# Optimization experiments

Measured on AMD Instinct MI355X. Metric: run time of the kernel, lower is better.

## Reference

```python
import jax, jax.numpy as jnp
import numpy as np

D = 128          # node_embedding_dim
R = 1024         # num_root_nodes
T = 4            # num trunk node types; encoder index T is the output autoencoder
OUT_SLOTS = 256  # num_output_nodes
START = T        # output_node_types_start
L = 64           # topological levels after the roots
M = 2048         # nodes per level
N = R + L * M    # total nodes = 132096


def setup_inputs() -> dict:
    key = jax.random.key(0)
    ks = jax.random.split(key, 4)
    rng = np.random.default_rng(0)
    # DAG by topological level: node in level l (1-based) reads parents with index < R + (l-1)*M
    hi = np.repeat(R + np.arange(L) * M, M)  # (N-R,) exclusive upper bound per node
    par = (rng.random((N - R, 2)) * hi[:, None]).astype(np.int64)
    is_out = rng.random(N - R) < 0.05
    types = rng.integers(0, T, N - R)
    types = np.where(is_out, START + rng.integers(0, OUT_SLOTS, N - R), types).astype(np.int64)
    s = 1.0 / np.sqrt(2 * D)
    return {
        "root_node_embeddings": jax.random.normal(ks[0], (R, D), jnp.float32),
        "W1": jax.random.normal(ks[1], (T + 1, 2 * D, 2 * D), jnp.float32) * s,  # encoder layer 1 (in, out)
        "b1": jnp.zeros((T + 1, 2 * D), jnp.float32),
        "W2": jax.random.normal(ks[2], (T + 1, 2 * D, D), jnp.float32) * s,      # encoder layer 2
        "b2": jnp.zeros((T + 1, D), jnp.float32),
        "out_slot_emb": jax.random.normal(ks[3], (OUT_SLOTS, D), jnp.float32),   # output_node_embeddings.weight
        "node_inputs_indices": jnp.asarray(par),  # (N-R, 2)
        "node_types": jnp.asarray(types),         # (N-R,)
    }


def _evaluate_graph(root, W1, b1, W2, b2, slots, par_idx, types):
    buf0 = jnp.zeros((N, D), root.dtype).at[:R].set(root)
    par_l = par_idx.reshape(L, M, 2)
    typ_l = types.reshape(L, M)
    m_ar = jnp.arange(M)

    def level_step(buf, inp):
        l, par, t = inp                        # par: (M,2) parent indices, t: (M,) node types
        is_out = t >= START
        e_idx = jnp.where(is_out, T, t)        # which autoencoder per node
        slot = jnp.clip(t - START, 0, OUT_SLOTS - 1)
        p = buf[par]                           # (M, 2, D) gather parent embeddings
        # output nodes use [parent0, slot_embedding] as encode input
        p1 = jnp.where(is_out[:, None], slots[slot], p[:, 1])
        x = jnp.concatenate([p[:, 0], p1], axis=-1)  # (M, 2D) flattened encoder input
        # run all T+1 tiny encoders, pick each node's type (cheap: weights are tiny)
        h_all = jnp.einsum('mi,tio->tmo', x, W1) + b1[:, None, :]  # (T+1, M, 2D)
        h = jax.nn.gelu(h_all[e_idx, m_ar], approximate=False)     # (M, 2D) exact GELU (torch default)
        e_all = jnp.einsum('mi,tio->tmo', h, W2) + b2[:, None, :]  # (T+1, M, D)
        e = e_all[e_idx, m_ar]                                     # (M, D)
        buf = jax.lax.dynamic_update_slice(buf, e, (R + l * M, 0))  # scatter level results
        return buf, None

    buf, _ = jax.lax.scan(level_step, buf0, (jnp.arange(L), par_l, typ_l))
    return buf


_evaluate_graph_jit = jax.jit(_evaluate_graph)


def reference(root_node_embeddings, W1, b1, W2, b2, out_slot_emb, node_inputs_indices, node_types):
    return _evaluate_graph_jit(root_node_embeddings, W1, b1, W2, b2, out_slot_emb,
                               node_inputs_indices, node_types)
```

## Files before the change

### kernel.cpp

```cpp
#include <hip/hip_runtime.h>
#include <math.h>

#define DD 128
#define RR 1024
#define TT 4
#define LL 64
#define MM 2048
#define NBK 16
#define GT 37
#define GO 10
#define CCAP (4*GT + GO)
#define PAD16 (CCAP*NBK)
#define CH CCAP
#define SENTU 0xFFFFFFFFu

typedef __attribute__((ext_vector_type(8))) short short8v;
typedef __attribute__((ext_vector_type(4))) float f32x4;

static __device__ __forceinline__ unsigned short f2bf(float f) {
    unsigned u = __float_as_uint(f);
    unsigned r = (u + 0x7fffu + ((u >> 16) & 1u)) >> 16;
    return (unsigned short)r;
}

static __device__ __forceinline__ float gelu_f(float h) {
    float x  = h * 0.70710678118654752f;
    float ax = fabsf(x);
    float t  = __builtin_amdgcn_rcpf(fmaf(0.3275911f, ax, 1.0f));
    float p  = fmaf(t, 1.061405429f, -1.453152027f);
    p = fmaf(p, t, 1.421413741f);
    p = fmaf(p, t, -0.284496736f);
    p = fmaf(p, t, 0.254829592f);
    p = p * t;
    float er = 1.0f - p * __expf(-ax * ax);
    er = copysignf(er, x);
    return 0.5f * h * (1.0f + er);
}

__global__ __launch_bounds__(256) void prep_all(
    const float* __restrict__ root, const float* __restrict__ W1,
    const float* __restrict__ W2, const int* __restrict__ types,
    const int* __restrict__ par,
    float* __restrict__ buf,
    unsigned short* __restrict__ W1F, unsigned short* __restrict__ W2F,
    unsigned short* __restrict__ order)
{
    int bid = blockIdx.x, tid = threadIdx.x;
    if (bid < LL) {
        int l = bid;
        __shared__ int cnt[10], cur[10];
        if (tid < 10) cnt[tid] = 0;
        __syncthreads();
        for (int s = tid; s < PAD16; s += 256) order[l*PAD16 + s] = 0xFFFFu;
        int thr = RR + (l-1)*MM;
        for (int m = tid; m < MM; m += 256) {
            int gi = l*MM + m;
            int t = types[gi];
            int e = (t >= TT) ? TT : t;
            int p0 = par[2*gi];
            bool rec = (p0 >= RR) && (p0 >= thr);
            if (t < TT) {
                int p1 = par[2*gi + 1];
                rec = rec || ((p1 >= RR) && (p1 >= thr));
            }
            atomicAdd(&cnt[e*2 + (rec ? 1 : 0)], 1);
        }
        __syncthreads();
        if (tid == 0) {
            for (int e = 0; e < 5; e++) {
                int base = ((e < 4) ? e*GT : 4*GT) * NBK;
                int s = cnt[e*2];
                cur[e*2]     = base;
                cur[e*2 + 1] = base + ((s + NBK - 1)/NBK)*NBK;
            }
        }
        __syncthreads();
        for (int m = tid; m < MM; m += 256) {
            int gi = l*MM + m;
            int t = types[gi];
            int e = (t >= TT) ? TT : t;
            int p0 = par[2*gi];
            bool rec = (p0 >= RR) && (p0 >= thr);
            if (t < TT) {
                int p1 = par[2*gi + 1];
                rec = rec || ((p1 >= RR) && (p1 >= thr));
            }
            int pos = atomicAdd(&cur[e*2 + (rec ? 1 : 0)], 1);
            order[l*PAD16 + pos] = (unsigned short)m;
        }
    } else if (bid < LL + 240) {
        int t0 = (bid - LL)*256 + tid;
        if (t0 < 5*16*8*64) {
            int lane = t0 & 63;
            int kk = (t0 >> 6) & 7;
            int nt = (t0 >> 9) & 15;
            int e  = t0 >> 13;
            int n  = nt*16 + (lane & 15);
            int k0 = kk*32 + (lane >> 4)*8;
            unsigned short v[8];
            #pragma unroll
            for (int j = 0; j < 8; j++) v[j] = f2bf(W1[(e*256 + k0 + j)*256 + n]);
            *(short8v*)&W1F[t0*8] = *(short8v*)v;
        } else {
            int t = t0 - 5*16*8*64;
            int lane = t & 63;
            int kk = (t >> 6) & 7;
            int nt = (t >> 9) & 7;
            int e  = t >> 12;
            int n  = nt*16 + (lane & 15);
            int k0 = kk*32 + (lane >> 4)*8;
            unsigned short v[8];
            #pragma unroll
            for (int j = 0; j < 8; j++) v[j] = f2bf(W2[(e*256 + k0 + j)*128 + n]);
            *(short8v*)&W2F[t*8] = *(short8v*)v;
        }
    } else if (bid < LL + 240 + 32) {
        int idx = (bid - (LL + 240))*256 + tid;
        const f32x4* r4 = (const f32x4*)root;
        f32x4* o4 = (f32x4*)buf;
        #pragma unroll
        for (int q = 0; q < 4; q++) o4[idx*4 + q] = r4[idx*4 + q];
    } else {
        int idx = (bid - (LL + 240 + 32))*256 + tid;
        float s = __uint_as_float(SENTU);
        f32x4 sv = (f32x4){s, s, s, s};
        f32x4* p = (f32x4*)(buf + (size_t)RR*DD) + (size_t)idx*4;
        p[0] = sv; p[1] = sv; p[2] = sv; p[3] = sv;
    }
}

__global__ __launch_bounds__(512, 2) void persist_mfma(
    const unsigned short* __restrict__ W1F, const unsigned short* __restrict__ W2F,
    const float* __restrict__ b1, const float* __restrict__ b2,
    const float* __restrict__ slots, const int* __restrict__ par,
    const int* __restrict__ types, const unsigned short* __restrict__ order,
    float* __restrict__ buf)
{
    __shared__ int4 descs[LL][NBK];
    __shared__ int ech[LL];
    __shared__ unsigned short axFA[8*64*8];
    __shared__ unsigned short axFB[8*64*8];
    __shared__ unsigned short hxF[8*64*8];

    int tid = threadIdx.x;
    int wg  = blockIdx.x;
    int e_wg = (wg < 4*GT) ? (wg / GT) : TT;

    int w  = tid >> 6;
    int lq = tid & 63;
    int m_own   = tid >> 4;
    int seg_own = tid & 15;

    short8v w1r0[8], w1r1[8], w2r[8];
    #pragma unroll
    for (int kk = 0; kk < 8; kk++) {
        w1r0[kk] = *(const short8v*)&W1F[(((e_wg*16 + 2*w + 0)*8 + kk)*64 + lq)*8];
        w1r1[kk] = *(const short8v*)&W1F[(((e_wg*16 + 2*w + 1)*8 + kk)*64 + lq)*8];
        w2r[kk]  = *(const short8v*)&W2F[(((e_wg*8  + w)*8 + kk)*64 + lq)*8];
    }
    float b1v0 = b1[e_wg*256 + (2*w + 0)*16 + (lq & 15)];
    float b1v1 = b1[e_wg*256 + (2*w + 1)*16 + (lq & 15)];
    float b2v  = b2[e_wg*128 + w*16 + (lq & 15)];

    for (int i = tid; i < LL*NBK; i += 512) {
        int l = i >> 4, s = i & 15;
        unsigned short o = order[l*PAD16 + wg*NBK + s];
        int4 d;
        if (o == 0xFFFFu) {
            d = make_int4(-1, 0, 0, -1);
        } else {
            int gi = l*MM + (int)o;
            int t = types[gi];
            int e = (t >= TT) ? TT : t;
            int p0 = par[2*gi];
            int p1 = (t >= TT) ? ~(t - TT) : par[2*gi + 1];
            d = make_int4((int)o, p0, p1, e);
        }
        descs[l][s] = d;
    }
    __syncthreads();
    for (int i = tid; i < LL; i += 512) ech[i] = descs[i][0].w;
    __syncthreads();

    #define RESOLVE_SRC(l1, S, P) {                                            \
        int4 d_ = descs[l1][m_own];                                            \
        if (d_.x < 0) { P = true; S = nullptr; }                               \
        else {                                                                 \
            P = false;                                                         \
            if (seg_own < 8)   S = buf + (size_t)d_.y*DD + seg_own*16;         \
            else if (d_.z < 0) S = slots + (size_t)(~d_.z)*DD + (seg_own-8)*16;\
            else               S = buf + (size_t)d_.z*DD + (seg_own-8)*16;     \
        } }

    #define LOAD8(S, U) {                                                      \
        const unsigned long long* s8_ = (const unsigned long long*)(S);        \
        _Pragma("unroll")                                                      \
        for (int q_ = 0; q_ < 8; q_++)                                         \
            U[q_] = __hip_atomic_load(&s8_[q_], __ATOMIC_RELAXED,              \
                                      __HIP_MEMORY_SCOPE_AGENT);               \
    }

    #define VERIFY(U, OK) { OK = true;                                         \
        _Pragma("unroll")                                                      \
        for (int q_ = 0; q_ < 8; q_++) {                                       \
            unsigned lo_ = (unsigned)U[q_], hi_ = (unsigned)(U[q_] >> 32);     \
            OK = OK && (lo_ != SENTU) && (hi_ != SENTU);                       \
        } }

    #define WRITE_FRAGS_U(AXT, U) {                                            \
        unsigned short tA_[8], tB_[8];                                         \
        _Pragma("unroll")                                                      \
        for (int q_ = 0; q_ < 4; q_++) {                                       \
            tA_[2*q_]   = f2bf(__uint_as_float((unsigned)U[q_]));              \
            tA_[2*q_+1] = f2bf(__uint_as_float((unsigned)(U[q_] >> 32)));      \
            tB_[2*q_]   = f2bf(__uint_as_float((unsigned)U[4+q_]));            \
            tB_[2*q_+1] = f2bf(__uint_as_float((unsigned)(U[4+q_] >> 32)));    \
        }                                                                      \
        int k_ = seg_own*16;                                                   \
        int kk_ = k_ >> 5, ln_ = m_own + 16*((k_ >> 3) & 3);                   \
        *(short8v*)&AXT[(kk_*64 + ln_)*8] = *(short8v*)tA_;                    \
        k_ += 8; kk_ = k_ >> 5; ln_ = m_own + 16*((k_ >> 3) & 3);              \
        *(short8v*)&AXT[(kk_*64 + ln_)*8] = *(short8v*)tB_;                    \
    }

    if (tid < 256) {
        const float* src; bool pad;
        RESOLVE_SRC(0, src, pad);
        unsigned long long u0[8];
        if (!pad) {
            LOAD8(src, u0);
            bool ok; VERIFY(u0, ok);
            while (!ok) { __builtin_amdgcn_s_sleep(1); LOAD8(src, u0); VERIFY(u0, ok); }
        } else {
            #pragma unroll
            for (int q = 0; q < 8; q++) u0[q] = 0ull;
        }
        WRITE_FRAGS_U(axFA, u0);
    }
    __syncthreads();

    unsigned short* axc = axFA;
    unsigned short* axn = axFB;

    for (int l = 0; l < LL; l++) {
        bool havN = (l + 1 < LL);

        const float* srcN = nullptr; bool padN = true; bool ok = true;
        unsigned long long u[8];
        #pragma unroll
        for (int q = 0; q < 8; q++) u[q] = 0ull;
        if (havN && tid < 256) {
            RESOLVE_SRC(l+1, srcN, padN);
            if (!padN) { LOAD8(srcN, u); ok = false; }
        }
        __builtin_amdgcn_sched_barrier(0);

        int e = ech[l];
        if (e >= 0) {
            f32x4 acc0 = (f32x4){b1v0, b1v0, b1v0, b1v0};
            f32x4 acc1 = (f32x4){b1v1, b1v1, b1v1, b1v1};
            {
                const short8v* Ab = (const short8v*)axc;
                #pragma unroll
                for (int kk = 0; kk < 8; kk++) {
                    short8v a = Ab[kk*64 + lq];
                    acc0 = __builtin_amdgcn_mfma_f32_16x16x32_bf16(a, w1r0[kk], acc0, 0, 0, 0);
                    acc1 = __builtin_amdgcn_mfma_f32_16x16x32_bf16(a, w1r1[kk], acc1, 0, 0, 0);
                }
            }
            if (havN && tid < 256 && !padN && !ok) {
                VERIFY(u, ok);
                if (!ok) LOAD8(srcN, u);
            }
            __builtin_amdgcn_sched_barrier(0);

            #pragma unroll
            for (int c = 0; c < 2; c++) {
                int nh = (2*w + c)*16 + (lq & 15);
                int kk2 = nh >> 5;
                int jj  = nh & 7;
                int lhi = 16*((nh >> 3) & 3);
                #pragma unroll
                for (int r = 0; r < 4; r++) {
                    int m = (lq >> 4)*4 + r;
                    float h = (c == 0) ? acc0[r] : acc1[r];
                    hxF[(kk2*64 + (m + lhi))*8 + jj] = f2bf(gelu_f(h));
                }
            }
            __syncthreads();

            f32x4 acc2 = (f32x4){b2v, b2v, b2v, b2v};
            {
                const short8v* Hb = (const short8v*)hxF;
                #pragma unroll
                for (int kk = 0; kk < 8; kk++) {
                    short8v a = Hb[kk*64 + lq];
                    acc2 = __builtin_amdgcn_mfma_f32_16x16x32_bf16(a, w2r[kk], acc2, 0, 0, 0);
                }
            }
            int baserow = RR + l*MM;
            int n = w*16 + (lq & 15);
            #pragma unroll
            for (int r = 0; r < 4; r++) {
                int m = (lq >> 4)*4 + r;
                int node = descs[l][m].x;
                if (node >= 0)
                    __hip_atomic_store(&buf[(size_t)(baserow + node)*DD + n], acc2[r],
                                       __ATOMIC_RELAXED, __HIP_MEMORY_SCOPE_AGENT);
            }
            if (havN && tid < 256 && !padN && !ok) {
                VERIFY(u, ok);
                if (!ok) LOAD8(srcN, u);
            }
        }

        if (havN && tid < 256) {
            if (!padN) {
                while (!ok) {
                    VERIFY(u, ok);
                    if (!ok) { __builtin_amdgcn_s_sleep(1); LOAD8(srcN, u); }
                }
            }
            WRITE_FRAGS_U(axn, u);
        }

        __syncthreads();
        unsigned short* t2 = axc; axc = axn; axn = t2;
    }
}

extern "C" void kernel_launch(void* const* d_in, const int* in_sizes, int n_in,
                              void* d_out, int out_size, void* d_ws, size_t ws_size,
                              hipStream_t stream) {
    const float* root  = (const float*)d_in[0];
    const float* W1    = (const float*)d_in[1];
    const float* b1    = (const float*)d_in[2];
    const float* W2    = (const float*)d_in[3];
    const float* b2    = (const float*)d_in[4];
    const float* slots = (const float*)d_in[5];
    const int*   par   = (const int*)d_in[6];
    const int*   typ   = (const int*)d_in[7];
    float* out = (float*)d_out;

    unsigned short* W1F   = (unsigned short*)d_ws;
    unsigned short* W2F   = W1F + 5*16*8*64*8;
    unsigned short* order = W2F + 5*8*8*64*8;

    prep_all<<<LL + 240 + 32 + 4096, 256, 0, stream>>>(root, W1, W2, typ, par, out,
                                                       W1F, W2F, order);

    void* args[] = { (void*)&W1F, (void*)&W2F, (void*)&b1, (void*)&b2,
                     (void*)&slots, (void*)&par, (void*)&typ, (void*)&order,
                     (void*)&out };
    hipLaunchCooperativeKernel((const void*)persist_mfma, dim3(CH), dim3(512),
                               args, 0, stream);
}
```

Measured before the change: 244.0 us.

## Fuse prep into persistent kernel with grid barrier; split gathers and MFMA chains

The separate prep kernel (level ordering, weight bf16 repacking, root copy, sentinel fill) is folded into the cooperative persistent kernel, with a hand-rolled atomic grid barrier replacing the kernel boundary. This removes one launch and its gap, at the cost of a memset and a spin barrier. The parent-embedding gather now uses all 512 threads with 4x8-byte loads each, instead of 256 threads with 8 loads. The dependent MFMA accumulation chains are split into four independent accumulators that are summed afterward, to shorten the serial latency per level.

Result: slower. 304.5 us (+24.8%).

```diff
diff --git a/kernel.cpp b/kernel.cpp
--- a/kernel.cpp
+++ b/kernel.cpp
@@ -13,9 +13,16 @@
 #define PAD16 (CCAP*NBK)
 #define CH CCAP
 #define SENTU 0xFFFFFFFFu
+#define SENTU8 0xFFFFFFFFFFFFFFFFull
+
+#define ITW1 (5*16*8*64)
+#define ITW2 (ITW1 + 5*8*8*64)
+#define ITRT (ITW2 + 8192)
+#define ITSN (ITRT + 1048576)
 
 typedef __attribute__((ext_vector_type(8))) short short8v;
 typedef __attribute__((ext_vector_type(4))) float f32x4;
+typedef unsigned long long ull;
 
 static __device__ __forceinline__ unsigned short f2bf(float f) {
     unsigned u = __float_as_uint(f);
@@ -37,23 +44,41 @@
     return 0.5f * h * (1.0f + er);
 }
 
-__global__ __launch_bounds__(256) void prep_all(
+static __device__ __forceinline__ void st8(void* p, ull v) {
+    __hip_atomic_store((ull*)p, v, __ATOMIC_RELAXED, __HIP_MEMORY_SCOPE_AGENT);
+}
+static __device__ __forceinline__ ull ld8(const void* p) {
+    return __hip_atomic_load((const ull*)p, __ATOMIC_RELAXED, __HIP_MEMORY_SCOPE_AGENT);
+}
+
+__global__ __launch_bounds__(512, 2) void persist_all(
     const float* __restrict__ root, const float* __restrict__ W1,
-    const float* __restrict__ W2, const int* __restrict__ types,
-    const int* __restrict__ par,
+    const float* __restrict__ b1, const float* __restrict__ W2,
+    const float* __restrict__ b2, const float* __restrict__ slots,
+    const int* __restrict__ par, const int* __restrict__ types,
     float* __restrict__ buf,
     unsigned short* __restrict__ W1F, unsigned short* __restrict__ W2F,
-    unsigned short* __restrict__ order)
+    unsigned short* __restrict__ order, int* __restrict__ barmem)
 {
-    int bid = blockIdx.x, tid = threadIdx.x;
-    if (bid < LL) {
-        int l = bid;
-        __shared__ int cnt[10], cur[10];
+    __shared__ int4 descs[LL][NBK];
+    __shared__ int ech[LL];
+    __shared__ unsigned short axFA[8*64*8];
+    __shared__ unsigned short axFB[8*64*8];
+    __shared__ unsigned short hxF[8*64*8];
+    __shared__ unsigned short order_l[PAD16];
+    __shared__ int cnt[10], cur[10];
+
+    int tid = threadIdx.x;
+    int wg  = blockIdx.x;
+    int e_wg = (wg < 4*GT) ? (wg / GT) : TT;
+
+    if (wg < LL) {
+        int l = wg;
         if (tid < 10) cnt[tid] = 0;
         __syncthreads();
-        for (int s = tid; s < PAD16; s += 256) order[l*PAD16 + s] = 0xFFFFu;
+        for (int s = tid; s < PAD16; s += 512) order_l[s] = 0xFFFFu;
         int thr = RR + (l-1)*MM;
-        for (int m = tid; m < MM; m += 256) {
+        for (int m = tid; m < MM; m += 512) {
             int gi = l*MM + m;
             int t = types[gi];
             int e = (t >= TT) ? TT : t;
@@ -75,7 +100,7 @@
             }
         }
         __syncthreads();
-        for (int m = tid; m < MM; m += 256) {
+        for (int m = tid; m < MM; m += 512) {
             int gi = l*MM + m;
             int t = types[gi];
             int e = (t >= TT) ? TT : t;
@@ -86,11 +111,16 @@
                 rec = rec || ((p1 >= RR) && (p1 >= thr));
             }
             int pos = atomicAdd(&cur[e*2 + (rec ? 1 : 0)], 1);
-            order[l*PAD16 + pos] = (unsigned short)m;
-        }
-    } else if (bid < LL + 240) {
-        int t0 = (bid - LL)*256 + tid;
-        if (t0 < 5*16*8*64) {
+            order_l[pos] = (unsigned short)m;
+        }
+        __syncthreads();
+        const ull* ol = (const ull*)order_l;
+        ull* og = (ull*)(order + (size_t)l*PAD16);
+        for (int i = tid; i < PAD16/4; i += 512) st8(&og[i], ol[i]);
+    }
+    for (long it = (long)wg*512 + tid; it < ITSN; it += (long)CH*512) {
+        if (it < ITW1) {
+            int t0 = (int)it;
             int lane = t0 & 63;
             int kk = (t0 >> 6) & 7;
             int nt = (t0 >> 9) & 15;
@@ -100,9 +130,11 @@
             unsigned short v[8];
             #pragma unroll
             for (int j = 0; j < 8; j++) v[j] = f2bf(W1[(e*256 + k0 + j)*256 + n]);
-            *(short8v*)&W1F[t0*8] = *(short8v*)v;
-        } else {
-            int t = t0 - 5*16*8*64;
+            ull* d = (ull*)&W1F[(size_t)t0*8];
+            st8(&d[0], ((const ull*)v)[0]);
+            st8(&d[1], ((const ull*)v)[1]);
+        } else if (it < ITW2) {
+            int t = (int)(it - ITW1);
             int lane = t & 63;
             int kk = (t >> 6) & 7;
             int nt = (t >> 9) & 7;
@@ -112,44 +144,43 @@
             unsigned short v[8];
             #pragma unroll
             for (int j = 0; j < 8; j++) v[j] = f2bf(W2[(e*256 + k0 + j)*128 + n]);
-            *(short8v*)&W2F[t*8] = *(short8v*)v;
-        }
-    } else if (bid < LL + 240 + 32) {
-        int idx = (bid - (LL + 240))*256 + tid;
-        const f32x4* r4 = (const f32x4*)root;
-        f32x4* o4 = (f32x4*)buf;
-        #pragma unroll
-        for (int q = 0; q < 4; q++) o4[idx*4 + q] = r4[idx*4 + q];
-    } else {
-        int idx = (bid - (LL + 240 + 32))*256 + tid;
-        float s = __uint_as_float(SENTU);
-        f32x4 sv = (f32x4){s, s, s, s};
-        f32x4* p = (f32x4*)(buf + (size_t)RR*DD) + (size_t)idx*4;
-        p[0] = sv; p[1] = sv; p[2] = sv; p[3] = sv;
-    }
-}
-
-__global__ __launch_bounds__(512, 2) void persist_mfma(
-    const unsigned short* __restrict__ W1F, const unsigned short* __restrict__ W2F,
-    const float* __restrict__ b1, const float* __restrict__ b2,
-    const float* __restrict__ slots, const int* __restrict__ par,
-    const int* __restrict__ types, const unsigned short* __restrict__ order,
-    float* __restrict__ buf)
-{
-    __shared__ int4 descs[LL][NBK];
-    __shared__ int ech[LL];
-    __shared__ unsigned short axFA[8*64*8];
-    __shared__ unsigned short axFB[8*64*8];
-    __shared__ unsigned short hxF[8*64*8];
-
-    int tid = threadIdx.x;
-    int wg  = blockIdx.x;
-    int e_wg = (wg < 4*GT) ? (wg / GT) : TT;
+            ull* d = (ull*)&W2F[(size_t)t*8];
+            st8(&d[0], ((const ull*)v)[0]);
+            st8(&d[1], ((const ull*)v)[1]);
+        } else if (it < ITRT) {
+            int i = (int)(it - ITW2);
+            const ull* s = (const ull*)(root + (size_t)i*16);
+            ull* d = (ull*)(buf + (size_t)i*16);
+            #pragma unroll
+            for (int q = 0; q < 8; q++) st8(&d[q], s[q]);
+        } else {
+            long i = it - ITRT;
+            ull* d = (ull*)(buf + (size_t)RR*DD + i*16);
+            #pragma unroll
+            for (int q = 0; q < 8; q++) st8(&d[q], SENTU8);
+        }
+    }
+    asm volatile("s_waitcnt vmcnt(0)" ::: "memory");
+    __syncthreads();
+    if (tid == 0) {
+        int old = __hip_atomic_fetch_add(barmem, 1, __ATOMIC_RELAXED, __HIP_MEMORY_SCOPE_AGENT);
+        if (old == CH - 1) {
+            __hip_atomic_store(barmem + 32, 1, __ATOMIC_RELAXED, __HIP_MEMORY_SCOPE_AGENT);
+        } else {
+            while (__hip_atomic_load(barmem + 32, __ATOMIC_RELAXED, __HIP_MEMORY_SCOPE_AGENT) == 0)
+                __builtin_amdgcn_s_sleep(2);
+        }
+    }
+    __syncthreads();
 
     int w  = tid >> 6;
     int lq = tid & 63;
-    int m_own   = tid >> 4;
-    int seg_own = tid & 15;
+    int m_own   = tid >> 5;
+    int hs      = tid & 31;
+    int kk_own  = hs >> 2;
+    int lane_own = m_own + 16*(hs & 3);
+    int seg16   = hs >> 1;
+    int half8   = hs & 1;
 
     short8v w1r0[8], w1r1[8], w2r[8];
     #pragma unroll
@@ -164,7 +195,7 @@
 
     for (int i = tid; i < LL*NBK; i += 512) {
         int l = i >> 4, s = i & 15;
-        unsigned short o = order[l*PAD16 + wg*NBK + s];
+        unsigned short o = order[(size_t)l*PAD16 + wg*NBK + s];
         int4 d;
         if (o == 0xFFFFu) {
             d = make_int4(-1, 0, 0, -1);
@@ -187,55 +218,50 @@
         if (d_.x < 0) { P = true; S = nullptr; }                               \
         else {                                                                 \
             P = false;                                                         \
-            if (seg_own < 8)   S = buf + (size_t)d_.y*DD + seg_own*16;         \
-            else if (d_.z < 0) S = slots + (size_t)(~d_.z)*DD + (seg_own-8)*16;\
-            else               S = buf + (size_t)d_.z*DD + (seg_own-8)*16;     \
+            if (seg16 < 8)     S = buf + (size_t)d_.y*DD + seg16*16 + half8*8; \
+            else if (d_.z < 0) S = slots + (size_t)(~d_.z)*DD + (seg16-8)*16 + half8*8; \
+            else               S = buf + (size_t)d_.z*DD + (seg16-8)*16 + half8*8; \
         } }
 
-    #define LOAD8(S, U) {                                                      \
-        const unsigned long long* s8_ = (const unsigned long long*)(S);        \
+    #define LOAD4P(S, U) {                                                     \
+        const ull* s8_ = (const ull*)(S);                                      \
         _Pragma("unroll")                                                      \
-        for (int q_ = 0; q_ < 8; q_++)                                         \
-            U[q_] = __hip_atomic_load(&s8_[q_], __ATOMIC_RELAXED,              \
-                                      __HIP_MEMORY_SCOPE_AGENT);               \
-    }
-
-    #define VERIFY(U, OK) { OK = true;                                         \
+        for (int q_ = 0; q_ < 4; q_++) U[q_] = s8_[q_];                        \
+    }
+    #define LOAD4(S, U) {                                                      \
+        const ull* s8_ = (const ull*)(S);                                      \
         _Pragma("unroll")                                                      \
-        for (int q_ = 0; q_ < 8; q_++) {                                       \
+        for (int q_ = 0; q_ < 4; q_++) U[q_] = ld8(&s8_[q_]);                  \
+    }
+    #define VERIFY4(U, OK) { OK = true;                                        \
+        _Pragma("unroll")                                                      \
+        for (int q_ = 0; q_ < 4; q_++) {                                       \
             unsigned lo_ = (unsigned)U[q_], hi_ = (unsigned)(U[q_] >> 32);     \
             OK = OK && (lo_ != SENTU) && (hi_ != SENTU);                       \
         } }
-
-    #define WRITE_FRAGS_U(AXT, U) {                                            \
-        unsigned short tA_[8], tB_[8];                                         \
+    #define WRITE_FRAG1(AXT, U) {                                              \
+        unsigned short t_[8];                                                  \
         _Pragma("unroll")                                                      \
         for (int q_ = 0; q_ < 4; q_++) {                                       \
-            tA_[2*q_]   = f2bf(__uint_as_float((unsigned)U[q_]));              \
-            tA_[2*q_+1] = f2bf(__uint_as_float((unsigned)(U[q_] >> 32)));      \
-            tB_[2*q_]   = f2bf(__uint_as_float((unsigned)U[4+q_]));            \
-            tB_[2*q_+1] = f2bf(__uint_as_float((unsigned)(U[4+q_] >> 32)));    \
+            t_[2*q_]   = f2bf(__uint_as_float((unsigned)U[q_]));               \
+            t_[2*q_+1] = f2bf(__uint_as_float((unsigned)(U[q_] >> 32)));       \
         }                                                                      \
-        int k_ = seg_own*16;                                                   \
-        int kk_ = k_ >> 5, ln_ = m_own + 16*((k_ >> 3) & 3);                   \
-        *(short8v*)&AXT[(kk_*64 + ln_)*8] = *(short8v*)tA_;                    \
-        k_ += 8; kk_ = k_ >> 5; ln_ = m_own + 16*((k_ >> 3) & 3);              \
-        *(short8v*)&AXT[(kk_*64 + ln_)*8] = *(short8v*)tB_;                    \
-    }
-
-    if (tid < 256) {
+        *(short8v*)&AXT[(kk_own*64 + lane_own)*8] = *(short8v*)t_;             \
+    }
+
+    {
         const float* src; bool pad;
         RESOLVE_SRC(0, src, pad);
-        unsigned long long u0[8];
+        ull u0[4];
         if (!pad) {
-            LOAD8(src, u0);
-            bool ok; VERIFY(u0, ok);
-            while (!ok) { __builtin_amdgcn_s_sleep(1); LOAD8(src, u0); VERIFY(u0, ok); }
+            LOAD4P(src, u0);
+            bool ok; VERIFY4(u0, ok);
+            while (!ok) { __builtin_amdgcn_s_sleep(1); LOAD4(src, u0); VERIFY4(u0, ok); }
         } else {
             #pragma unroll
-            for (int q = 0; q < 8; q++) u0[q] = 0ull;
-        }
-        WRITE_FRAGS_U(axFA, u0);
+            for (int q = 0; q < 4; q++) u0[q] = 0ull;
+        }
+        WRITE_FRAG1(axFA, u0);
     }
     __syncthreads();
 
@@ -246,31 +272,46 @@
         bool havN = (l + 1 < LL);
 
         const float* srcN = nullptr; bool padN = true; bool ok = true;
-        unsigned long long u[8];
+        ull u[4];
         #pragma unroll
-        for (int q = 0; q < 8; q++) u[q] = 0ull;
-        if (havN && tid < 256) {
+        for (int q = 0; q < 4; q++) u[q] = 0ull;
+        if (havN) {
             RESOLVE_SRC(l+1, srcN, padN);
-            if (!padN) { LOAD8(srcN, u); ok = false; }
+            if (!padN) { LOAD4P(srcN, u); ok = false; }
         }
         __builtin_amdgcn_sched_barrier(0);
 
         int e = ech[l];
         if (e >= 0) {
-            f32x4 acc0 = (f32x4){b1v0, b1v0, b1v0, b1v0};
-            f32x4 acc1 = (f32x4){b1v1, b1v1, b1v1, b1v1};
+            f32x4 z4 = (f32x4){0.f,0.f,0.f,0.f};
+            f32x4 a00 = (f32x4){b1v0,b1v0,b1v0,b1v0}, a01 = z4, a02 = z4, a03 = z4;
+            f32x4 a10 = (f32x4){b1v1,b1v1,b1v1,b1v1}, a11 = z4, a12 = z4, a13 = z4;
             {
                 const short8v* Ab = (const short8v*)axc;
-                #pragma unroll
-                for (int kk = 0; kk < 8; kk++) {
-                    short8v a = Ab[kk*64 + lq];
-                    acc0 = __builtin_amdgcn_mfma_f32_16x16x32_bf16(a, w1r0[kk], acc0, 0, 0, 0);
-                    acc1 = __builtin_amdgcn_mfma_f32_16x16x32_bf16(a, w1r1[kk], acc1, 0, 0, 0);
-                }
-            }
-            if (havN && tid < 256 && !padN && !ok) {
-                VERIFY(u, ok);
-                if (!ok) LOAD8(srcN, u);
+                short8v a0 = Ab[0*64+lq], a1 = Ab[1*64+lq], a2 = Ab[2*64+lq], a3 = Ab[3*64+lq];
+                short8v a4 = Ab[4*64+lq], a5 = Ab[5*64+lq], a6 = Ab[6*64+lq], a7 = Ab[7*64+lq];
+                a00 = __builtin_amdgcn_mfma_f32_16x16x32_bf16(a0, w1r0[0], a00, 0,0,0);
+                a01 = __builtin_amdgcn_mfma_f32_16x16x32_bf16(a2, w1r0[2], a01, 0,0,0);
+                a02 = __builtin_amdgcn_mfma_f32_16x16x32_bf16(a4, w1r0[4], a02, 0,0,0);
+                a03 = __builtin_amdgcn_mfma_f32_16x16x32_bf16(a6, w1r0[6], a03, 0,0,0);
+                a10 = __builtin_amdgcn_mfma_f32_16x16x32_bf16(a0, w1r1[0], a10, 0,0,0);
+                a11 = __builtin_amdgcn_mfma_f32_16x16x32_bf16(a2, w1r1[2], a11, 0,0,0);
+                a12 = __builtin_amdgcn_mfma_f32_16x16x32_bf16(a4, w1r1[4], a12, 0,0,0);
+                a13 = __builtin_amdgcn_mfma_f32_16x16x32_bf16(a6, w1r1[6], a13, 0,0,0);
+                a00 = __builtin_amdgcn_mfma_f32_16x16x32_bf16(a1, w1r0[1], a00, 0,0,0);
+                a01 = __builtin_amdgcn_mfma_f32_16x16x32_bf16(a3, w1r0[3], a01, 0,0,0);
+                a02 = __builtin_amdgcn_mfma_f32_16x16x32_bf16(a5, w1r0[5], a02, 0,0,0);
+                a03 = __builtin_amdgcn_mfma_f32_16x16x32_bf16(a7, w1r0[7], a03, 0,0,0);
+                a10 = __builtin_amdgcn_mfma_f32_16x16x32_bf16(a1, w1r1[1], a10, 0,0,0);
+                a11 = __builtin_amdgcn_mfma_f32_16x16x32_bf16(a3, w1r1[3], a11, 0,0,0);
+                a12 = __builtin_amdgcn_mfma_f32_16x16x32_bf16(a5, w1r1[5], a12, 0,0,0);
+                a13 = __builtin_amdgcn_mfma_f32_16x16x32_bf16(a7, w1r1[7], a13, 0,0,0);
+            }
+            f32x4 acc0 = (a00 + a01) + (a02 + a03);
+            f32x4 acc1 = (a10 + a11) + (a12 + a13);
+            if (havN && !padN && !ok) {
+                VERIFY4(u, ok);
+                if (!ok) LOAD4(srcN, u);
             }
             __builtin_amdgcn_sched_barrier(0);
 
@@ -289,15 +330,22 @@
             }
             __syncthreads();
 
-            f32x4 acc2 = (f32x4){b2v, b2v, b2v, b2v};
+            f32x4 z4b = (f32x4){0.f,0.f,0.f,0.f};
+            f32x4 c0 = (f32x4){b2v,b2v,b2v,b2v}, c1 = z4b, c2 = z4b, c3 = z4b;
             {
                 const short8v* Hb = (const short8v*)hxF;
-                #pragma unroll
-                for (int kk = 0; kk < 8; kk++) {
-                    short8v a = Hb[kk*64 + lq];
-                    acc2 = __builtin_amdgcn_mfma_f32_16x16x32_bf16(a, w2r[kk], acc2, 0, 0, 0);
-                }
-            }
+                short8v h0 = Hb[0*64+lq], h1 = Hb[1*64+lq], h2 = Hb[2*64+lq], h3 = Hb[3*64+lq];
+                short8v h4 = Hb[4*64+lq], h5 = Hb[5*64+lq], h6 = Hb[6*64+lq], h7 = Hb[7*64+lq];
+                c0 = __builtin_amdgcn_mfma_f32_16x16x32_bf16(h0, w2r[0], c0, 0,0,0);
+                c1 = __builtin_amdgcn_mfma_f32_16x16x32_bf16(h2, w2r[2], c1, 0,0,0);
+                c2 = __builtin_amdgcn_mfma_f32_16x16x32_bf16(h4, w2r[4], c2, 0,0,0);
+                c3 = __builtin_amdgcn_mfma_f32_16x16x32_bf16(h6, w2r[6], c3, 0,0,0);
+                c0 = __builtin_amdgcn_mfma_f32_16x16x32_bf16(h1, w2r[1], c0, 0,0,0);
+                c1 = __builtin_amdgcn_mfma_f32_16x16x32_bf16(h3, w2r[3], c1, 0,0,0);
+                c2 = __builtin_amdgcn_mfma_f32_16x16x32_bf16(h5, w2r[5], c2, 0,0,0);
+                c3 = __builtin_amdgcn_mfma_f32_16x16x32_bf16(h7, w2r[7], c3, 0,0,0);
+            }
+            f32x4 acc2 = (c0 + c1) + (c2 + c3);
             int baserow = RR + l*MM;
             int n = w*16 + (lq & 15);
             #pragma unroll
@@ -308,20 +356,20 @@
                     __hip_atomic_store(&buf[(size_t)(baserow + node)*DD + n], acc2[r],
                                        __ATOMIC_RELAXED, __HIP_MEMORY_SCOPE_AGENT);
             }
-            if (havN && tid < 256 && !padN && !ok) {
-                VERIFY(u, ok);
-                if (!ok) LOAD8(srcN, u);
-            }
-        }
-
-        if (havN && tid < 256) {
+            if (havN && !padN && !ok) {
+                VERIFY4(u, ok);
+                if (!ok) LOAD4(srcN, u);
+            }
+        }
+
+        if (havN) {
             if (!padN) {
                 while (!ok) {
-                    VERIFY(u, ok);
-                    if (!ok) { __builtin_amdgcn_s_sleep(1); LOAD8(srcN, u); }
+                    VERIFY4(u, ok);
+                    if (!ok) { __builtin_amdgcn_s_sleep(1); LOAD4(srcN, u); }
                 }
             }
-            WRITE_FRAGS_U(axn, u);
+            WRITE_FRAG1(axn, u);
         }
 
         __syncthreads();
@@ -345,13 +393,14 @@
     unsigned short* W1F   = (unsigned short*)d_ws;
     unsigned short* W2F   = W1F + 5*16*8*64*8;
     unsigned short* order = W2F + 5*8*8*64*8;
-
-    prep_all<<<LL + 240 + 32 + 4096, 256, 0, stream>>>(root, W1, W2, typ, par, out,
-                                                       W1F, W2F, order);
-
-    void* args[] = { (void*)&W1F, (void*)&W2F, (void*)&b1, (void*)&b2,
-                     (void*)&slots, (void*)&par, (void*)&typ, (void*)&order,
-                     (void*)&out };
-    hipLaunchCooperativeKernel((const void*)persist_mfma, dim3(CH), dim3(512),
+    int* barmem = (int*)(order + (size_t)LL*PAD16);
+
+    hipMemsetAsync(barmem, 0, 64*sizeof(int), stream);
+
+    void* args[] = { (void*)&root, (void*)&W1, (void*)&b1, (void*)&W2,
+                     (void*)&b2, (void*)&slots, (void*)&par, (void*)&typ,
+                     (void*)&out, (void*)&W1F, (void*)&W2F, (void*)&order,
+                     (void*)&barmem };
+    hipLaunchCooperativeKernel((const void*)persist_all, dim3(CH), dim3(512),
                                args, 0, stream);
 }
```
